# Kernel optimization log

Measured on AMD Instinct MI355X. Metric: run time of the kernel, lower is better.

Reference implementation:

```python
import jax, jax.numpy as jnp
import numpy as np

B, S, D, H = 4, 2048, 512, 16
HD = D // H          # head_dim = 32
ROPE_DIM = HD        # rope_pct = 1.0
NEG = -1e30


def apply_rope(x):
    # x: [B, H, S, HD]; rotate first ROPE_DIM dims, half-split (NeoX) convention
    half = ROPE_DIM // 2
    pos = jnp.arange(S, dtype=jnp.float32)
    inv_freq = 1.0 / (10000.0 ** (jnp.arange(0, ROPE_DIM, 2, dtype=jnp.float32) / ROPE_DIM))
    ang = pos[:, None] * inv_freq[None, :]          # [S, half]
    cos, sin = jnp.cos(ang), jnp.sin(ang)           # broadcast over B,H
    x1 = x[..., :half]
    x2 = x[..., half:ROPE_DIM]
    r1 = x1 * cos - x2 * sin
    r2 = x2 * cos + x1 * sin
    rest = x[..., ROPE_DIM:]
    return jnp.concatenate([r1, r2, rest], axis=-1)


def setup_inputs() -> dict:
    key = jax.random.key(0)
    ks = jax.random.split(key, 7)
    x = jax.random.normal(ks[0], (B, S, D), dtype=jnp.float32)
    # causal mask: True = block (j > i)
    attn_mask = jnp.triu(jnp.ones((S, S), dtype=bool), k=1)
    # padding mask: True = PAD; random lengths in [S//2, S]
    lengths = jax.random.randint(ks[1], (B,), S // 2, S + 1)
    key_padding_mask = jnp.arange(S)[None, :] >= lengths[:, None]
    scale = D ** -0.5
    Wq = jax.random.normal(ks[2], (D, D), dtype=jnp.float32) * scale
    Wk = jax.random.normal(ks[3], (D, D), dtype=jnp.float32) * scale
    Wv = jax.random.normal(ks[4], (D, D), dtype=jnp.float32) * scale
    Wo = jax.random.normal(ks[5], (D, D), dtype=jnp.float32) * scale
    return {"x": x, "attn_mask": attn_mask, "key_padding_mask": key_padding_mask,
            "Wq": Wq, "Wk": Wk, "Wv": Wv, "Wo": Wo}


def reference(x, attn_mask, key_padding_mask, Wq, Wk, Wv, Wo):
    scale = HD ** -0.5
    # nn.Linear: y = x @ W.T
    q = (x @ Wq.T).reshape(B, S, H, HD).transpose(0, 2, 1, 3)  # [B,H,S,HD]
    k = (x @ Wk.T).reshape(B, S, H, HD).transpose(0, 2, 1, 3)
    v = (x @ Wv.T).reshape(B, S, H, HD).transpose(0, 2, 1, 3)
    q = apply_rope(q)
    k = apply_rope(k)
    scores = jnp.einsum('bhid,bhjd->bhij', q, k) * scale       # [B,H,S,S]
    scores = jnp.where(key_padding_mask[:, None, None, :], NEG, scores)
    scores = jnp.where(attn_mask[None, None, :, :], NEG, scores)
    probs = jax.nn.softmax(scores.astype(jnp.float32), axis=-1)
    probs = jnp.nan_to_num(probs, nan=0.0)
    ctx = jnp.einsum('bhij,bhjd->bhid', probs, v)              # [B,H,S,HD]
    ctx = ctx.transpose(0, 2, 1, 3).reshape(B, S, D)
    ctx = jnp.where(key_padding_mask[:, :, None], 0.0, ctx)
    return ctx @ Wo.T
```

## Files before the change

kernel.cpp:

```cpp
#include <hip/hip_runtime.h>
#include <hip/hip_bf16.h>

#define B_ 4
#define S_ 2048
#define D_ 512
#define H_ 16
#define HD_ 32

typedef __bf16 bf16;
typedef __bf16 bf16x4 __attribute__((ext_vector_type(4)));
typedef __bf16 bf16x8 __attribute__((ext_vector_type(8)));
typedef float f32x4 __attribute__((ext_vector_type(4)));

__device__ __forceinline__ f32x4 mfma16(bf16x8 a, bf16x8 b, f32x4 c) {
  return __builtin_amdgcn_mfma_f32_16x16x32_bf16(a, b, c, 0, 0, 0);
}

__device__ __forceinline__ void gload16(const bf16* g, bf16* l) {
  __builtin_amdgcn_global_load_lds(
      (const __attribute__((address_space(1))) void*)g,
      (__attribute__((address_space(3))) void*)l, 16, 0, 0);
}

__device__ __forceinline__ bf16x8 cvt8(const float* __restrict__ p) {
  const f32x4* v = (const f32x4*)p;
  f32x4 a = v[0], b = v[1];
  bf16x8 r;
  r[0] = (bf16)a[0]; r[1] = (bf16)a[1]; r[2] = (bf16)a[2]; r[3] = (bf16)a[3];
  r[4] = (bf16)b[0]; r[5] = (bf16)b[1]; r[6] = (bf16)b[2]; r[7] = (bf16)b[3];
  return r;
}

__global__ __launch_bounds__(256) void prep_kernel(
    const float* __restrict__ x, const float* __restrict__ wq,
    const float* __restrict__ wk, const float* __restrict__ wv,
    const float* __restrict__ wo, const unsigned char* __restrict__ am,
    const unsigned char* __restrict__ kpm, bf16* __restrict__ xb,
    bf16* __restrict__ dq, bf16* __restrict__ dk, bf16* __restrict__ dv,
    bf16* __restrict__ dwo, int* __restrict__ lengths_out) {
  int bid = blockIdx.x;
  if (bid < 2048) {
    size_t i = (size_t)bid * 256 + threadIdx.x;
    *(bf16x8*)(xb + i * 8) = cvt8(x + i * 8);
  } else if (bid < 2560) {
    int wb = bid - 2048;
    int mat = wb >> 7;
    size_t i = (size_t)(wb & 127) * 256 + threadIdx.x;
    const float* s = (mat == 0) ? wq : (mat == 1) ? wk : (mat == 2) ? wv : wo;
    bf16* d = (mat == 0) ? dq : (mat == 1) ? dk : (mat == 2) ? dv : dwo;
    *(bf16x8*)(d + i * 8) = cvt8(s + i * 8);
  } else {
    int b = threadIdx.x >> 6, lane = threadIdx.x & 63;
    int esize;
    if (am[1] == 1) esize = 1;
    else if (am[2] == 0x80 && am[3] == 0x3F) esize = 2;
    else if (am[3] == 0x3C) esize = 2;
    else if (am[4] == 1) esize = 4;
    else if (am[6] == 0x80 && am[7] == 0x3F) esize = 4;
    else if (am[8] == 1) esize = 8;
    else esize = 1;
    int cnt = 0;
    for (int i = lane; i < S_; i += 64) {
      size_t off = ((size_t)b * S_ + i) * (size_t)esize;
      unsigned char nz = 0;
      for (int e = 0; e < esize; ++e) nz |= kpm[off + e];
      cnt += (nz == 0) ? 1 : 0;
    }
    for (int off = 1; off < 64; off <<= 1) cnt += __shfl_xor(cnt, off);
    if (lane == 0) lengths_out[b] = cnt;
  }
}

#define LDT 136
__global__ __launch_bounds__(256) void qkv_rope_kernel(
    const bf16* __restrict__ x,
    const bf16* __restrict__ Wq, const bf16* __restrict__ Wk,
    const bf16* __restrict__ Wv,
    bf16* __restrict__ q_ws,
    bf16* __restrict__ k_ws,
    bf16* __restrict__ vt_ws)
{
  __shared__ __align__(16) bf16 smem[17408];
#define AS(b) (smem + (b) * 4096)
#define BS(b) (smem + 8192 + (b) * 4096)
#define CT smem

  int bid = blockIdx.x;
  int brow = bid / 12, bc = bid % 12;
  int mat = bc >> 2;
  const bf16* W = (mat == 0) ? Wq : (mat == 1) ? Wk : Wv;
  int row0 = brow * 128;
  int col0 = (bc & 3) * 128;

  int tid = threadIdx.x;
  int w = tid >> 6, l = tid & 63;
  int wr = w >> 1, wc = w & 1;
  int g = l >> 4, c = l & 15;
  int lrow = l >> 2;
  int lcol = (l & 3) * 8;

  f32x4 acc[4][4];
  f32x4 zero = {0.f, 0.f, 0.f, 0.f};
#pragma unroll
  for (int m = 0; m < 4; ++m)
#pragma unroll
    for (int n = 0; n < 4; ++n) acc[m][n] = zero;

#pragma unroll
  for (int j = 0; j < 2; ++j) {
    int chunk = w * 2 + j;
    int grow = chunk * 16 + lrow;
    gload16(x + (size_t)(row0 + grow) * 512 + lcol, AS(0) + chunk * 512);
    gload16(W + (size_t)(col0 + grow) * 512 + lcol, BS(0) + chunk * 512);
  }
  __syncthreads();
  int cur = 0;

#pragma unroll 1
  for (int k0 = 0; k0 < 512; k0 += 32) {
    bool more = (k0 < 480);
    if (more) {
#pragma unroll
      for (int j = 0; j < 2; ++j) {
        int chunk = w * 2 + j;
        int grow = chunk * 16 + lrow;
        gload16(x + (size_t)(row0 + grow) * 512 + k0 + 32 + lcol,
                AS(cur ^ 1) + chunk * 512);
        gload16(W + (size_t)(col0 + grow) * 512 + k0 + 32 + lcol,
                BS(cur ^ 1) + chunk * 512);
      }
    }
    bf16x8 af[4], bfr[4];
#pragma unroll
    for (int m = 0; m < 4; ++m)
      af[m] = *(const bf16x8*)(AS(cur) + (wr * 64 + m * 16 + c) * 32 + g * 8);
#pragma unroll
    for (int n = 0; n < 4; ++n)
      bfr[n] = *(const bf16x8*)(BS(cur) + (wc * 64 + n * 16 + c) * 32 + g * 8);
#pragma unroll
    for (int m = 0; m < 4; ++m)
#pragma unroll
      for (int n = 0; n < 4; ++n) acc[m][n] = mfma16(af[m], bfr[n], acc[m][n]);
    if (more) {
      __syncthreads();
      cur ^= 1;
    }
  }

  if (mat < 2) {
    bf16* dst = (mat == 0) ? q_ws : k_ws;
    float invf = powf(10000.0f, -(float)c * (1.0f / 16.0f));
#pragma unroll
    for (int m = 0; m < 4; ++m) {
      int rbase = row0 + wr * 64 + m * 16 + g * 4;
#pragma unroll
      for (int r = 0; r < 4; ++r) {
        int grow = rbase + r;
        int bb = grow >> 11, s = grow & (S_ - 1);
        float ang = (float)s * invf;
        float cs = cosf(ang), sn = sinf(ang);
#pragma unroll
        for (int np = 0; np < 2; ++np) {
          int n = np * 2;
          int obase = col0 + wc * 64 + n * 16;
          int h = obase >> 5;
          float a0 = acc[m][n][r], a1 = acc[m][n + 1][r];
          size_t base = (((size_t)bb * H_ + h) * S_ + s) * HD_;
          dst[base + c] = (bf16)(a0 * cs - a1 * sn);
          dst[base + c + 16] = (bf16)(a1 * cs + a0 * sn);
        }
      }
    }
  } else {
    __syncthreads();
#pragma unroll
    for (int m = 0; m < 4; ++m) {
#pragma unroll
      for (int n = 0; n < 4; ++n) {
        int o = wc * 64 + n * 16 + c;
        int sb = wr * 64 + m * 16 + g * 4;
        bf16x4 q4;
        q4[0] = (bf16)acc[m][n][0]; q4[1] = (bf16)acc[m][n][1];
        q4[2] = (bf16)acc[m][n][2]; q4[3] = (bf16)acc[m][n][3];
        *(bf16x4*)(&CT[o * LDT + sb]) = q4;
      }
    }
    __syncthreads();
    int o_l = tid >> 1, sh = (tid & 1) * 64;
    int o = col0 + o_l;
    int h = o >> 5, hd = o & 31;
    int bb2 = row0 >> 11, sr = row0 & (S_ - 1);
    size_t dst = (((size_t)bb2 * H_ + h) * HD_ + hd) * S_ + sr + sh;
#pragma unroll
    for (int j = 0; j < 8; ++j)
      *(bf16x8*)(vt_ws + dst + j * 8) =
          *(const bf16x8*)(&CT[o_l * LDT + sh + j * 8]);
  }
#undef AS
#undef BS
#undef CT
}

#define LDK2 40
#define LDV 72
#define LDP 72
__global__ __launch_bounds__(256) void attn_kernel(
    const bf16* __restrict__ q_ws, const bf16* __restrict__ k_ws,
    const bf16* __restrict__ vt_ws, const int* __restrict__ lengths,
    bf16* __restrict__ ctx_ws)
{
  __shared__ __align__(16) bf16 Ks[2][64 * LDK2];
  __shared__ __align__(16) bf16 Vts[2][HD_ * LDV];
  __shared__ __align__(16) bf16 Ps[4][16 * LDP];

  int p = blockIdx.x;
  int bh = blockIdx.y;
  int bb = bh >> 4, h = bh & 15;
  int tid = threadIdx.x, w = tid >> 6, l = tid & 63, g = l >> 4, c = l & 15;
  const size_t bh_base = ((size_t)bb * H_ + h) * (size_t)S_ * HD_;
  const float escale = 0.17677669529663687f * 1.4426950408889634f;
  int len = lengths[bb];
  int rowrel = w * 16 + c;

  int srowK = tid >> 2, skgK = tid & 3;
  int srowV = tid >> 3, ssgV = tid & 7;

#pragma unroll 1
  for (int phase = 0; phase < 2; ++phase) {
    int qt = phase ? (31 - p) : p;
    int q0 = qt * 64 + w * 16;

    bf16x8 qf = *(const bf16x8*)(q_ws + bh_base + (size_t)(q0 + c) * HD_ + g * 8);

    f32x4 zero = {0.f, 0.f, 0.f, 0.f};
    f32x4 ctxa[2];
    ctxa[0] = zero; ctxa[1] = zero;
    float lrun = 0.f;

    bf16x8 regK = *(const bf16x8*)(k_ws + bh_base + (size_t)srowK * HD_ + skgK * 8);
    bf16x8 regV = *(const bf16x8*)(vt_ws + bh_base + (size_t)srowV * S_ + ssgV * 8);
    __syncthreads();
    *(bf16x8*)(&Ks[0][srowK * LDK2 + skgK * 8]) = regK;
    *(bf16x8*)(&Vts[0][srowV * LDV + ssgV * 8]) = regV;
    __syncthreads();
    int cur = 0;

#pragma unroll 1
    for (int kt = 0; kt <= qt; ++kt) {
      bool hasNext = (kt < qt);
      if (hasNext) {
        regK = *(const bf16x8*)(k_ws + bh_base +
                                (size_t)((kt + 1) * 64 + srowK) * HD_ + skgK * 8);
        regV = *(const bf16x8*)(vt_ws + bh_base + (size_t)srowV * S_ +
                                (kt + 1) * 64 + ssgV * 8);
      }
      const bf16* KsC = Ks[cur];
      const bf16* VtsC = Vts[cur];

      f32x4 sacc[4];
#pragma unroll
      for (int n = 0; n < 4; ++n) {
        bf16x8 kf = *(const bf16x8*)(&KsC[(n * 16 + c) * LDK2 + g * 8]);
        sacc[n] = mfma16(kf, qf, zero);
      }

      float sv[4][4];
      if (kt != qt) {
#pragma unroll
        for (int n = 0; n < 4; ++n)
#pragma unroll
          for (int r = 0; r < 4; ++r)
            sv[n][r] = __builtin_amdgcn_exp2f(sacc[n][r] * escale);
      } else {
#pragma unroll
        for (int n = 0; n < 4; ++n) {
          int jr = n * 16 + g * 4;
#pragma unroll
          for (int r = 0; r < 4; ++r) {
            float e = __builtin_amdgcn_exp2f(sacc[n][r] * escale);
            sv[n][r] = (jr + r > rowrel) ? 0.f : e;
          }
        }
      }
#pragma unroll
      for (int n = 0; n < 4; ++n)
        lrun += (sv[n][0] + sv[n][1]) + (sv[n][2] + sv[n][3]);

#pragma unroll
      for (int n = 0; n < 4; ++n) {
        bf16x4 pk;
        pk[0] = (bf16)sv[n][0]; pk[1] = (bf16)sv[n][1];
        pk[2] = (bf16)sv[n][2]; pk[3] = (bf16)sv[n][3];
        *(bf16x4*)(&Ps[w][c * LDP + n * 16 + g * 4]) = pk;
      }

      bf16x8 pf0 = *(const bf16x8*)(&Ps[w][c * LDP + g * 8]);
      bf16x8 pf1 = *(const bf16x8*)(&Ps[w][c * LDP + 32 + g * 8]);
#pragma unroll
      for (int n = 0; n < 2; ++n) {
        bf16x8 v0 = *(const bf16x8*)(&VtsC[(n * 16 + c) * LDV + g * 8]);
        bf16x8 v1 = *(const bf16x8*)(&VtsC[(n * 16 + c) * LDV + 32 + g * 8]);
        ctxa[n] = mfma16(pf0, v0, ctxa[n]);
        ctxa[n] = mfma16(pf1, v1, ctxa[n]);
      }

      if (hasNext) {
        *(bf16x8*)(&Ks[cur ^ 1][srowK * LDK2 + skgK * 8]) = regK;
        *(bf16x8*)(&Vts[cur ^ 1][srowV * LDV + ssgV * 8]) = regV;
        __syncthreads();
        cur ^= 1;
      }
    }

    float tot = lrun + __shfl_xor(lrun, 16);
    tot += __shfl_xor(tot, 32);
    float lr[4];
#pragma unroll
    for (int r = 0; r < 4; ++r) lr[r] = __shfl(tot, g * 4 + r);
#pragma unroll
    for (int n = 0; n < 2; ++n)
#pragma unroll
      for (int r = 0; r < 4; ++r) {
        int qr = q0 + g * 4 + r;
        float val = ctxa[n][r] / lr[r];
        if (qr >= len) val = 0.f;
        ctx_ws[(((size_t)bb * S_ + qr) * H_ + h) * HD_ + n * 16 + c] = (bf16)val;
      }
  }
}

__global__ __launch_bounds__(256) void out_proj_kernel(
    const bf16* __restrict__ ctx, const bf16* __restrict__ Wo,
    float* __restrict__ out) {
  __shared__ __align__(16) bf16 As[2][4096];
  __shared__ __align__(16) bf16 Bs[2][4096];

  int bid = blockIdx.x;
  int brow = bid >> 2, bc = bid & 3;
  int row0 = brow * 128, col0 = bc * 128;
  int tid = threadIdx.x;
  int w = tid >> 6, l = tid & 63;
  int wr = w >> 1, wc = w & 1;
  int g = l >> 4, c = l & 15;
  int lrow = l >> 2;
  int lcol = (l & 3) * 8;

  f32x4 acc[4][4];
  f32x4 zero = {0.f, 0.f, 0.f, 0.f};
#pragma unroll
  for (int m = 0; m < 4; ++m)
#pragma unroll
    for (int n = 0; n < 4; ++n) acc[m][n] = zero;

#pragma unroll
  for (int j = 0; j < 2; ++j) {
    int chunk = w * 2 + j;
    int grow = chunk * 16 + lrow;
    gload16(ctx + (size_t)(row0 + grow) * 512 + lcol, As[0] + chunk * 512);
    gload16(Wo + (size_t)(col0 + grow) * 512 + lcol, Bs[0] + chunk * 512);
  }
  __syncthreads();
  int cur = 0;

#pragma unroll 1
  for (int k0 = 0; k0 < 512; k0 += 32) {
    bool more = (k0 < 480);
    if (more) {
#pragma unroll
      for (int j = 0; j < 2; ++j) {
        int chunk = w * 2 + j;
        int grow = chunk * 16 + lrow;
        gload16(ctx + (size_t)(row0 + grow) * 512 + k0 + 32 + lcol,
                As[cur ^ 1] + chunk * 512);
        gload16(Wo + (size_t)(col0 + grow) * 512 + k0 + 32 + lcol,
                Bs[cur ^ 1] + chunk * 512);
      }
    }
    bf16x8 af[4], bfr[4];
#pragma unroll
    for (int m = 0; m < 4; ++m)
      af[m] = *(const bf16x8*)(As[cur] + (wr * 64 + m * 16 + c) * 32 + g * 8);
#pragma unroll
    for (int n = 0; n < 4; ++n)
      bfr[n] = *(const bf16x8*)(Bs[cur] + (wc * 64 + n * 16 + c) * 32 + g * 8);
#pragma unroll
    for (int m = 0; m < 4; ++m)
#pragma unroll
      for (int n = 0; n < 4; ++n) acc[m][n] = mfma16(af[m], bfr[n], acc[m][n]);
    if (more) {
      __syncthreads();
      cur ^= 1;
    }
  }

#pragma unroll
  for (int m = 0; m < 4; ++m) {
    int rbase = row0 + wr * 64 + m * 16 + g * 4;
#pragma unroll
    for (int n = 0; n < 4; ++n) {
      int o = col0 + wc * 64 + n * 16 + c;
#pragma unroll
      for (int r = 0; r < 4; ++r)
        out[(size_t)(rbase + r) * 512 + o] = acc[m][n][r];
    }
  }
}

extern "C" void kernel_launch(void* const* d_in, const int* in_sizes, int n_in,
                              void* d_out, int out_size, void* d_ws,
                              size_t ws_size, hipStream_t stream) {
  const float* x = (const float*)d_in[0];
  const unsigned char* am = (const unsigned char*)d_in[1];
  const unsigned char* kpm = (const unsigned char*)d_in[2];
  const float* Wq = (const float*)d_in[3];
  const float* Wk = (const float*)d_in[4];
  const float* Wv = (const float*)d_in[5];
  const float* Wo = (const float*)d_in[6];
  float* out = (float*)d_out;

  char* ws = (char*)d_ws;
  int* lengths = (int*)ws;
  const size_t QKV_ELEMS = (size_t)B_ * H_ * S_ * HD_;
  const size_t W_ELEMS = (size_t)D_ * D_;
  bf16* xb = (bf16*)(ws + 256);
  bf16* q_ws = xb + QKV_ELEMS;
  bf16* k_ws = q_ws + QKV_ELEMS;
  bf16* vt_ws = k_ws + QKV_ELEMS;
  bf16* wqb = vt_ws + QKV_ELEMS;
  bf16* wkb = wqb + W_ELEMS;
  bf16* wvb = wkb + W_ELEMS;
  bf16* wob = wvb + W_ELEMS;
  bf16* ctx_ws = xb;

  hipLaunchKernelGGL(prep_kernel, dim3(2561), dim3(256), 0, stream, x, Wq, Wk,
                     Wv, Wo, am, kpm, xb, wqb, wkb, wvb, wob, lengths);
  hipLaunchKernelGGL(qkv_rope_kernel, dim3(768), dim3(256), 0, stream, xb, wqb,
                     wkb, wvb, q_ws, k_ws, vt_ws);
  hipLaunchKernelGGL(attn_kernel, dim3(16, 64), dim3(256), 0, stream, q_ws, k_ws,
                     vt_ws, lengths, ctx_ws);
  hipLaunchKernelGGL(out_proj_kernel, dim3(256), dim3(256), 0, stream, ctx_ws,
                     wob, out);
}
```

Baseline: 127.1 us.

## Precompute RoPE tables, fragment-ordered LDS layouts, MFMA row sums in attention

Adds RoPE cos/sin tables computed in the prep kernel, so the QKV epilogue does table loads instead of per-element powf/cosf/sinf. In the attention kernel, K, V^T and P tiles in LDS are stored in MFMA fragment order, so each lane reads a contiguous 16-byte slot without padded strides or bank conflicts. The softmax denominator is now accumulated by an MFMA against a ones vector rather than scalar adds plus shuffles. The trade-offs are extra workspace, extra prep blocks, and a row sum taken over bf16-rounded probabilities.

Result: slower. 130.8 us (+2.8%).

```diff
diff --git a/kernel.cpp b/kernel.cpp
--- a/kernel.cpp
+++ b/kernel.cpp
@@ -37,7 +37,8 @@
     const float* __restrict__ wo, const unsigned char* __restrict__ am,
     const unsigned char* __restrict__ kpm, bf16* __restrict__ xb,
     bf16* __restrict__ dq, bf16* __restrict__ dk, bf16* __restrict__ dv,
-    bf16* __restrict__ dwo, int* __restrict__ lengths_out) {
+    bf16* __restrict__ dwo, int* __restrict__ lengths_out,
+    float* __restrict__ costab, float* __restrict__ sintab) {
   int bid = blockIdx.x;
   if (bid < 2048) {
     size_t i = (size_t)bid * 256 + threadIdx.x;
@@ -49,7 +50,7 @@
     const float* s = (mat == 0) ? wq : (mat == 1) ? wk : (mat == 2) ? wv : wo;
     bf16* d = (mat == 0) ? dq : (mat == 1) ? dk : (mat == 2) ? dv : dwo;
     *(bf16x8*)(d + i * 8) = cvt8(s + i * 8);
-  } else {
+  } else if (bid == 2560) {
     int b = threadIdx.x >> 6, lane = threadIdx.x & 63;
     int esize;
     if (am[1] == 1) esize = 1;
@@ -68,18 +69,22 @@
     }
     for (int off = 1; off < 64; off <<= 1) cnt += __shfl_xor(cnt, off);
     if (lane == 0) lengths_out[b] = cnt;
+  } else {
+    int ti = (bid - 2561) * 256 + threadIdx.x;
+    int s = ti >> 4, cc = ti & 15;
+    float invf = powf(10000.0f, -(float)cc * (1.0f / 16.0f));
+    float ang = (float)s * invf;
+    costab[ti] = cosf(ang);
+    sintab[ti] = sinf(ang);
   }
 }
 
 #define LDT 136
 __global__ __launch_bounds__(256) void qkv_rope_kernel(
-    const bf16* __restrict__ x,
-    const bf16* __restrict__ Wq, const bf16* __restrict__ Wk,
-    const bf16* __restrict__ Wv,
-    bf16* __restrict__ q_ws,
-    bf16* __restrict__ k_ws,
-    bf16* __restrict__ vt_ws)
-{
+    const bf16* __restrict__ x, const bf16* __restrict__ Wq,
+    const bf16* __restrict__ Wk, const bf16* __restrict__ Wv,
+    const float* __restrict__ costab, const float* __restrict__ sintab,
+    bf16* __restrict__ q_ws, bf16* __restrict__ k_ws, bf16* __restrict__ vt_ws) {
   __shared__ __align__(16) bf16 smem[17408];
 #define AS(b) (smem + (b) * 4096)
 #define BS(b) (smem + 8192 + (b) * 4096)
@@ -149,7 +154,6 @@
 
   if (mat < 2) {
     bf16* dst = (mat == 0) ? q_ws : k_ws;
-    float invf = powf(10000.0f, -(float)c * (1.0f / 16.0f));
 #pragma unroll
     for (int m = 0; m < 4; ++m) {
       int rbase = row0 + wr * 64 + m * 16 + g * 4;
@@ -157,8 +161,8 @@
       for (int r = 0; r < 4; ++r) {
         int grow = rbase + r;
         int bb = grow >> 11, s = grow & (S_ - 1);
-        float ang = (float)s * invf;
-        float cs = cosf(ang), sn = sinf(ang);
+        float cs = costab[s * 16 + c];
+        float sn = sintab[s * 16 + c];
 #pragma unroll
         for (int np = 0; np < 2; ++np) {
           int n = np * 2;
@@ -201,17 +205,13 @@
 #undef CT
 }
 
-#define LDK2 40
-#define LDV 72
-#define LDP 72
 __global__ __launch_bounds__(256) void attn_kernel(
     const bf16* __restrict__ q_ws, const bf16* __restrict__ k_ws,
     const bf16* __restrict__ vt_ws, const int* __restrict__ lengths,
-    bf16* __restrict__ ctx_ws)
-{
-  __shared__ __align__(16) bf16 Ks[2][64 * LDK2];
-  __shared__ __align__(16) bf16 Vts[2][HD_ * LDV];
-  __shared__ __align__(16) bf16 Ps[4][16 * LDP];
+    bf16* __restrict__ ctx_ws) {
+  __shared__ __align__(16) bf16 Ks[2][2048];
+  __shared__ __align__(16) bf16 Vts[2][2048];
+  __shared__ __align__(16) bf16 Ps[4][1024];
 
   int p = blockIdx.x;
   int bh = blockIdx.y;
@@ -224,6 +224,14 @@
 
   int srowK = tid >> 2, skgK = tid & 3;
   int srowV = tid >> 3, ssgV = tid & 7;
+  int slotK8 = (skgK * 16 + (srowK & 15) + ((srowK >> 4) << 6)) * 8;
+  int slotV8 =
+      ((ssgV & 3) * 16 + (srowV & 15) + (((ssgV >> 2) + ((srowV >> 4) << 1)) << 6)) * 8;
+
+  bf16 one = (bf16)1.0f;
+  bf16x8 onesf;
+#pragma unroll
+  for (int i = 0; i < 8; ++i) onesf[i] = one;
 
 #pragma unroll 1
   for (int phase = 0; phase < 2; ++phase) {
@@ -235,13 +243,18 @@
     f32x4 zero = {0.f, 0.f, 0.f, 0.f};
     f32x4 ctxa[2];
     ctxa[0] = zero; ctxa[1] = zero;
-    float lrun = 0.f;
-
-    bf16x8 regK = *(const bf16x8*)(k_ws + bh_base + (size_t)srowK * HD_ + skgK * 8);
-    bf16x8 regV = *(const bf16x8*)(vt_ws + bh_base + (size_t)srowV * S_ + ssgV * 8);
+    f32x4 lsum = zero;
+
+    const bf16* kptr = k_ws + bh_base + (size_t)srowK * HD_ + skgK * 8;
+    const bf16* vptr = vt_ws + bh_base + (size_t)srowV * S_ + ssgV * 8;
+
+    bf16x8 regK = *(const bf16x8*)kptr;
+    bf16x8 regV = *(const bf16x8*)vptr;
+    kptr += 64 * HD_;
+    vptr += 64;
     __syncthreads();
-    *(bf16x8*)(&Ks[0][srowK * LDK2 + skgK * 8]) = regK;
-    *(bf16x8*)(&Vts[0][srowV * LDV + ssgV * 8]) = regV;
+    *(bf16x8*)(&Ks[0][slotK8]) = regK;
+    *(bf16x8*)(&Vts[0][slotV8]) = regV;
     __syncthreads();
     int cur = 0;
 
@@ -249,10 +262,10 @@
     for (int kt = 0; kt <= qt; ++kt) {
       bool hasNext = (kt < qt);
       if (hasNext) {
-        regK = *(const bf16x8*)(k_ws + bh_base +
-                                (size_t)((kt + 1) * 64 + srowK) * HD_ + skgK * 8);
-        regV = *(const bf16x8*)(vt_ws + bh_base + (size_t)srowV * S_ +
-                                (kt + 1) * 64 + ssgV * 8);
+        regK = *(const bf16x8*)kptr;
+        regV = *(const bf16x8*)vptr;
+        kptr += 64 * HD_;
+        vptr += 64;
       }
       const bf16* KsC = Ks[cur];
       const bf16* VtsC = Vts[cur];
@@ -260,7 +273,7 @@
       f32x4 sacc[4];
 #pragma unroll
       for (int n = 0; n < 4; ++n) {
-        bf16x8 kf = *(const bf16x8*)(&KsC[(n * 16 + c) * LDK2 + g * 8]);
+        bf16x8 kf = *(const bf16x8*)(&KsC[(l + (n << 6)) * 8]);
         sacc[n] = mfma16(kf, qf, zero);
       }
 
@@ -282,47 +295,45 @@
           }
         }
       }
-#pragma unroll
-      for (int n = 0; n < 4; ++n)
-        lrun += (sv[n][0] + sv[n][1]) + (sv[n][2] + sv[n][3]);
 
 #pragma unroll
       for (int n = 0; n < 4; ++n) {
         bf16x4 pk;
         pk[0] = (bf16)sv[n][0]; pk[1] = (bf16)sv[n][1];
         pk[2] = (bf16)sv[n][2]; pk[3] = (bf16)sv[n][3];
-        *(bf16x4*)(&Ps[w][c * LDP + n * 16 + g * 4]) = pk;
-      }
-
-      bf16x8 pf0 = *(const bf16x8*)(&Ps[w][c * LDP + g * 8]);
-      bf16x8 pf1 = *(const bf16x8*)(&Ps[w][c * LDP + 32 + g * 8]);
-#pragma unroll
-      for (int n = 0; n < 2; ++n) {
-        bf16x8 v0 = *(const bf16x8*)(&VtsC[(n * 16 + c) * LDV + g * 8]);
-        bf16x8 v1 = *(const bf16x8*)(&VtsC[(n * 16 + c) * LDV + 32 + g * 8]);
-        ctxa[n] = mfma16(pf0, v0, ctxa[n]);
-        ctxa[n] = mfma16(pf1, v1, ctxa[n]);
+        int chunk = 2 * n + (g >> 1);
+        int off = ((chunk >> 2) << 9) + ((chunk & 3) * 16 + c) * 8 + ((g & 1) << 2);
+        *(bf16x4*)(&Ps[w][off]) = pk;
+      }
+
+      bf16x8 pf0 = *(const bf16x8*)(&Ps[w][l * 8]);
+      bf16x8 pf1 = *(const bf16x8*)(&Ps[w][512 + l * 8]);
+
+      lsum = mfma16(pf0, onesf, lsum);
+      lsum = mfma16(pf1, onesf, lsum);
+
+#pragma unroll
+      for (int n2 = 0; n2 < 2; ++n2) {
+        bf16x8 v0 = *(const bf16x8*)(&VtsC[(l + ((2 * n2) << 6)) * 8]);
+        bf16x8 v1 = *(const bf16x8*)(&VtsC[(l + ((1 + 2 * n2) << 6)) * 8]);
+        ctxa[n2] = mfma16(pf0, v0, ctxa[n2]);
+        ctxa[n2] = mfma16(pf1, v1, ctxa[n2]);
       }
 
       if (hasNext) {
-        *(bf16x8*)(&Ks[cur ^ 1][srowK * LDK2 + skgK * 8]) = regK;
-        *(bf16x8*)(&Vts[cur ^ 1][srowV * LDV + ssgV * 8]) = regV;
+        *(bf16x8*)(&Ks[cur ^ 1][slotK8]) = regK;
+        *(bf16x8*)(&Vts[cur ^ 1][slotV8]) = regV;
         __syncthreads();
         cur ^= 1;
       }
     }
 
-    float tot = lrun + __shfl_xor(lrun, 16);
-    tot += __shfl_xor(tot, 32);
-    float lr[4];
-#pragma unroll
-    for (int r = 0; r < 4; ++r) lr[r] = __shfl(tot, g * 4 + r);
 #pragma unroll
     for (int n = 0; n < 2; ++n)
 #pragma unroll
       for (int r = 0; r < 4; ++r) {
         int qr = q0 + g * 4 + r;
-        float val = ctxa[n][r] / lr[r];
+        float val = ctxa[n][r] / lsum[r];
         if (qr >= len) val = 0.f;
         ctx_ws[(((size_t)bb * S_ + qr) * H_ + h) * HD_ + n * 16 + c] = (bf16)val;
       }
@@ -430,12 +441,15 @@
   bf16* wkb = wqb + W_ELEMS;
   bf16* wvb = wkb + W_ELEMS;
   bf16* wob = wvb + W_ELEMS;
+  float* costab = (float*)(wob + W_ELEMS);
+  float* sintab = costab + (size_t)S_ * 16;
   bf16* ctx_ws = xb;
 
-  hipLaunchKernelGGL(prep_kernel, dim3(2561), dim3(256), 0, stream, x, Wq, Wk,
-                     Wv, Wo, am, kpm, xb, wqb, wkb, wvb, wob, lengths);
+  hipLaunchKernelGGL(prep_kernel, dim3(2689), dim3(256), 0, stream, x, Wq, Wk,
+                     Wv, Wo, am, kpm, xb, wqb, wkb, wvb, wob, lengths, costab,
+                     sintab);
   hipLaunchKernelGGL(qkv_rope_kernel, dim3(768), dim3(256), 0, stream, xb, wqb,
-                     wkb, wvb, q_ws, k_ws, vt_ws);
+                     wkb, wvb, costab, sintab, q_ws, k_ws, vt_ws);
   hipLaunchKernelGGL(attn_kernel, dim3(16, 64), dim3(256), 0, stream, q_ws, k_ws,
                      vt_ws, lengths, ctx_ws);
   hipLaunchKernelGGL(out_proj_kernel, dim3(256), dim3(256), 0, stream, ctx_ws,
```
